# Kernel tuning notes

Measured on AMD Instinct MI355X. Metric: run time of the kernel, lower is better.

Reference implementation:

```python
import jax, jax.numpy as jnp
import numpy as np

B, N, D = 8, 2048, 1024

def setup_inputs() -> dict:
    key = jax.random.key(0)
    k1, k2, k3, k4 = jax.random.split(key, 4)
    q = jax.random.normal(k1, (B, N, D), dtype=jnp.float32)
    k = jax.random.normal(k2, (B, N, D), dtype=jnp.float32)
    v = jax.random.uniform(k3, (B, N, N), dtype=jnp.float32)
    # nn.Linear default init (kaiming-uniform-ish); scale is irrelevant for correctness
    bound = 1.0 / np.sqrt(D)
    W1 = jax.random.uniform(k4, (D, D), dtype=jnp.float32, minval=-bound, maxval=bound)
    b1 = jnp.zeros((D,), dtype=jnp.float32)
    return {"q": q, "k": k, "v": v, "W1": W1, "b1": b1}

def adj_normalization(adj):
    # D^{-1/2} A D^{-1/2} with rowsum clamped at 1; expressed as O(N^2)
    # broadcast scaling instead of the original's two diagonal bmms.
    rowsum = jnp.maximum(adj.sum(-1), 1.0)          # [B, N]
    d_inv_sqrt = rowsum ** -0.5                      # [B, N]
    return d_inv_sqrt[:, :, None] * adj * d_inv_sqrt[:, None, :]

def reference(q, k, v, W1, b1):
    # ff_layers == 1: q_out = linear1(q) (dropout is identity in eval);
    # k is unused because _fc returns (q_out, q_out).
    q_out = jnp.einsum('bnd,ed->bne', q, W1) + b1    # [B, N, D]
    attn = jnp.einsum('bnd,bmd->bnm', q_out, q_out)  # [B, N, N]
    # comb_mode == 2 (learn_n_norm): symmetric normalization of attn; v unused.
    output = adj_normalization(attn)
    return (output, attn)
```

## Files before the change

### kernel.cpp

```cpp
#include <hip/hip_runtime.h>

#define B_ 8
#define N_ 2048
#define D_ 1024

using u16 = unsigned short;
typedef __attribute__((ext_vector_type(8))) short short8;
typedef __attribute__((ext_vector_type(4))) float f32x4;
typedef __attribute__((ext_vector_type(4))) float float4v;
typedef __attribute__((ext_vector_type(4))) int int4v;

static __device__ __forceinline__ float bf2f(u16 h) {
  return __uint_as_float(((unsigned)h) << 16);
}
static __device__ __forceinline__ u16 f2bf(float f) {
  unsigned u = __float_as_uint(f);
  u += 0x7FFFu + ((u >> 16) & 1u);
  return (u16)(u >> 16);
}

static __device__ __forceinline__ void gload16(const void* g, void* l) {
  __builtin_amdgcn_global_load_lds((const __attribute__((address_space(1))) void*)g,
                                   (__attribute__((address_space(3))) void*)l, 16, 0, 0);
}

__global__ void cvt_f32_to_bf16(const float* __restrict__ in, u16* __restrict__ out, int n8) {
  const int stride = gridDim.x * blockDim.x;
  for (int i = blockIdx.x * blockDim.x + threadIdx.x; i < n8; i += stride) {
    const float4v* p = (const float4v*)in + (size_t)i * 2;
    float4v a = p[0], b = p[1];
    union { u16 h[8]; int4v v; } r;
    r.h[0] = f2bf(a.x); r.h[1] = f2bf(a.y); r.h[2] = f2bf(a.z); r.h[3] = f2bf(a.w);
    r.h[4] = f2bf(b.x); r.h[5] = f2bf(b.y); r.h[6] = f2bf(b.z); r.h[7] = f2bf(b.w);
    ((int4v*)out)[i] = r.v;
  }
}

__global__ __launch_bounds__(256, 2)
void gemm1_kernel(const u16* __restrict__ A, const u16* __restrict__ Bm,
                  const float* __restrict__ bias, u16* __restrict__ C,
                  int Nc, int K)
{
  const int lane = threadIdx.x & 63;
  const int wave = threadIdx.x >> 6;
  const int wr = wave >> 1, wc = wave & 1;
  const int tM = blockIdx.y << 7;
  const int tN = blockIdx.x << 7;

  __shared__ u16 As[128 * 32];
  __shared__ u16 Bs[128 * 32];

  const int srow = wave * 16 + (lane >> 2);
  const int scol = (lane & 3) * 8;
  const u16* ga0 = A  + (size_t)(tM + srow)      * K + scol;
  const u16* ga1 = A  + (size_t)(tM + srow + 64) * K + scol;
  const u16* gb0 = Bm + (size_t)(tN + srow)      * K + scol;
  const u16* gb1 = Bm + (size_t)(tN + srow + 64) * K + scol;
  u16* lA0 = As + wave * 512;
  u16* lA1 = As + 2048 + wave * 512;
  u16* lB0 = Bs + wave * 512;
  u16* lB1 = Bs + 2048 + wave * 512;

  f32x4 acc[4][4];
  #pragma unroll
  for (int m = 0; m < 4; ++m)
    #pragma unroll
    for (int n = 0; n < 4; ++n)
      acc[m][n] = (f32x4){0.f, 0.f, 0.f, 0.f};

  const int arow = wr * 64 + (lane & 15);
  const int brow = wc * 64 + (lane & 15);
  const int kblk = (lane >> 4) * 8;

  for (int k0 = 0; k0 < K; k0 += 32) {
    __syncthreads();
    gload16(ga0 + k0, lA0);
    gload16(ga1 + k0, lA1);
    gload16(gb0 + k0, lB0);
    gload16(gb1 + k0, lB1);
    asm volatile("s_waitcnt vmcnt(0)" ::: "memory");
    __syncthreads();

    short8 af[4], bfr[4];
    #pragma unroll
    for (int m = 0; m < 4; ++m)
      af[m] = *(const short8*)(As + (arow + m * 16) * 32 + kblk);
    #pragma unroll
    for (int n = 0; n < 4; ++n)
      bfr[n] = *(const short8*)(Bs + (brow + n * 16) * 32 + kblk);

    #pragma unroll
    for (int m = 0; m < 4; ++m)
      #pragma unroll
      for (int n = 0; n < 4; ++n)
        acc[m][n] = __builtin_amdgcn_mfma_f32_16x16x32_bf16(af[m], bfr[n], acc[m][n], 0, 0, 0);
  }

  const int r0 = tM + wr * 64 + (lane >> 4) * 4;
  const int c0 = tN + wc * 64 + (lane & 15);
  #pragma unroll
  for (int m = 0; m < 4; ++m)
    #pragma unroll
    for (int n = 0; n < 4; ++n) {
      const int col = c0 + n * 16;
      const float bv = bias[col];
      #pragma unroll
      for (int j = 0; j < 4; ++j)
        C[(size_t)(r0 + m * 16 + j) * Nc + col] = f2bf(acc[m][n][j] + bv);
    }
}

__global__ __launch_bounds__(256, 2)
void gemm2_fused(const u16* __restrict__ Qbase, const float* __restrict__ dinv,
                 float* __restrict__ attnBase, float* __restrict__ outBase)
{
  const int z = blockIdx.z;
  const u16* A = Qbase + (size_t)z * N_ * D_;
  const int lane = threadIdx.x & 63;
  const int wave = threadIdx.x >> 6;
  const int wr = wave >> 1, wc = wave & 1;
  const int tM = blockIdx.y << 7;
  const int tN = blockIdx.x << 7;

  __shared__ u16 As[128 * 32];
  __shared__ u16 Bs[128 * 32];

  const int srow = wave * 16 + (lane >> 2);
  const int scol = (lane & 3) * 8;
  const u16* ga0 = A + (size_t)(tM + srow)      * D_ + scol;
  const u16* ga1 = A + (size_t)(tM + srow + 64) * D_ + scol;
  const u16* gb0 = A + (size_t)(tN + srow)      * D_ + scol;
  const u16* gb1 = A + (size_t)(tN + srow + 64) * D_ + scol;
  u16* lA0 = As + wave * 512;
  u16* lA1 = As + 2048 + wave * 512;
  u16* lB0 = Bs + wave * 512;
  u16* lB1 = Bs + 2048 + wave * 512;

  f32x4 acc[4][4];
  #pragma unroll
  for (int m = 0; m < 4; ++m)
    #pragma unroll
    for (int n = 0; n < 4; ++n)
      acc[m][n] = (f32x4){0.f, 0.f, 0.f, 0.f};

  const int arow = wr * 64 + (lane & 15);
  const int brow = wc * 64 + (lane & 15);
  const int kblk = (lane >> 4) * 8;

  for (int k0 = 0; k0 < D_; k0 += 32) {
    __syncthreads();
    gload16(ga0 + k0, lA0);
    gload16(ga1 + k0, lA1);
    gload16(gb0 + k0, lB0);
    gload16(gb1 + k0, lB1);
    asm volatile("s_waitcnt vmcnt(0)" ::: "memory");
    __syncthreads();

    short8 af[4], bfr[4];
    #pragma unroll
    for (int m = 0; m < 4; ++m)
      af[m] = *(const short8*)(As + (arow + m * 16) * 32 + kblk);
    #pragma unroll
    for (int n = 0; n < 4; ++n)
      bfr[n] = *(const short8*)(Bs + (brow + n * 16) * 32 + kblk);

    #pragma unroll
    for (int m = 0; m < 4; ++m)
      #pragma unroll
      for (int n = 0; n < 4; ++n)
        acc[m][n] = __builtin_amdgcn_mfma_f32_16x16x32_bf16(af[m], bfr[n], acc[m][n], 0, 0, 0);
  }

  float* Cattn = attnBase + (size_t)z * N_ * N_;
  float* Cout  = outBase  + (size_t)z * N_ * N_;
  const float* dv = dinv + z * N_;

  const int r0 = tM + wr * 64 + (lane >> 4) * 4;
  const int c0 = tN + wc * 64 + (lane & 15);
  float di[4][4];
  #pragma unroll
  for (int m = 0; m < 4; ++m)
    #pragma unroll
    for (int j = 0; j < 4; ++j)
      di[m][j] = dv[r0 + m * 16 + j];

  #pragma unroll
  for (int m = 0; m < 4; ++m)
    #pragma unroll
    for (int n = 0; n < 4; ++n) {
      const int col = c0 + n * 16;
      const float dj = dv[col];
      #pragma unroll
      for (int j = 0; j < 4; ++j) {
        const size_t off = (size_t)(r0 + m * 16 + j) * N_ + col;
        const float a = acc[m][n][j];
        Cattn[off] = a;
        Cout[off]  = a * di[m][j] * dj;
      }
    }
}

__global__ void qsum_kernel(const float* __restrict__ q, float* __restrict__ qsum) {
  const int b   = blockIdx.z;
  const int d   = blockIdx.x * 256 + threadIdx.x;
  const int r0  = blockIdx.y * 256;
  const float* p = q + ((size_t)b * N_ + r0) * D_ + d;
  float acc = 0.f;
  for (int r = 0; r < 256; ++r) acc += p[(size_t)r * D_];
  atomicAdd(&qsum[b * D_ + d], acc);
}

__global__ void s_kernel(const float* __restrict__ qsum, const float* __restrict__ W1,
                         const float* __restrict__ b1, float* __restrict__ s) {
  const int idx = blockIdx.x * 256 + threadIdx.x;
  const int b = idx >> 10, e = idx & (D_ - 1);
  const int d0 = blockIdx.y * 256;
  const float4v* wp = (const float4v*)(W1 + (size_t)e * D_ + d0);
  const float4v* qp = (const float4v*)(qsum + b * D_ + d0);
  float acc = 0.f;
  #pragma unroll 4
  for (int t = 0; t < 64; ++t) {
    float4v w = wp[t], qv = qp[t];
    acc += w.x * qv.x + w.y * qv.y + w.z * qv.z + w.w * qv.w;
  }
  if (blockIdx.y == 0) acc += (float)N_ * b1[e];
  atomicAdd(&s[b * D_ + e], acc);
}

__global__ void t_kernel(const float* __restrict__ W1, const float* __restrict__ s,
                         float* __restrict__ tv) {
  const int idx = blockIdx.x * 256 + threadIdx.x;
  const int b = idx >> 10, d = idx & (D_ - 1);
  const int e0 = blockIdx.y * 256;
  const float* wp = W1 + (size_t)e0 * D_ + d;
  const float* sp = s + b * D_ + e0;
  float acc = 0.f;
  #pragma unroll 8
  for (int e = 0; e < 256; ++e) acc += wp[(size_t)e * D_] * sp[e];
  atomicAdd(&tv[b * D_ + d], acc);
}

__global__ void c_kernel(const float* __restrict__ b1, const float* __restrict__ s,
                         float* __restrict__ c) {
  const int b = blockIdx.x;
  const int tid = threadIdx.x;
  float acc = 0.f;
  #pragma unroll
  for (int t = 0; t < 4; ++t) {
    const int e = tid + t * 256;
    acc += b1[e] * s[b * D_ + e];
  }
  __shared__ float red[4];
  #pragma unroll
  for (int off = 32; off; off >>= 1) acc += __shfl_down(acc, off);
  if ((tid & 63) == 0) red[tid >> 6] = acc;
  __syncthreads();
  if (tid == 0) c[b] = red[0] + red[1] + red[2] + red[3];
}

__global__ void rowdinv_kernel(const float* __restrict__ q, const float* __restrict__ tv,
                               const float* __restrict__ c, float* __restrict__ dinv) {
  const int row  = blockIdx.x * 4 + (threadIdx.x >> 6);
  const int lane = threadIdx.x & 63;
  const int b    = row >> 11;
  const float4v* p  = (const float4v*)(q + (size_t)row * D_);
  const float4v* tp = (const float4v*)(tv + b * D_);
  float acc = 0.f;
  #pragma unroll
  for (int it = 0; it < 4; ++it) {
    float4v qv = p[it * 64 + lane];
    float4v tw = tp[it * 64 + lane];
    acc += qv.x * tw.x + qv.y * tw.y + qv.z * tw.z + qv.w * tw.w;
  }
  #pragma unroll
  for (int off = 32; off; off >>= 1) acc += __shfl_down(acc, off);
  if (lane == 0) dinv[row] = rsqrtf(fmaxf(acc + c[b], 1.0f));
}

extern "C" void kernel_launch(void* const* d_in, const int* in_sizes, int n_in,
                              void* d_out, int out_size, void* d_ws, size_t ws_size,
                              hipStream_t stream) {
  const float* q  = (const float*)d_in[0];
  const float* W1 = (const float*)d_in[3];
  const float* b1 = (const float*)d_in[4];

  float* out  = (float*)d_out;
  float* attn = out + (size_t)B_ * N_ * N_;

  char* ws = (char*)d_ws;
  u16*   qbf  = (u16*)ws;
  u16*   qout = (u16*)(ws + (size_t)33554432);
  u16*   w1bf = (u16*)(ws + (size_t)67108864);
  float* qsum = (float*)(ws + (size_t)69206016);
  float* s    = (float*)(ws + (size_t)69238784);
  float* tv   = (float*)(ws + (size_t)69271552);
  float* c    = (float*)(ws + (size_t)69304320);
  float* dinv = (float*)(ws + (size_t)69304576);

  hipMemsetAsync(qsum, 0, 3 * B_ * D_ * sizeof(float) + 256, stream);

  cvt_f32_to_bf16<<<2048, 256, 0, stream>>>(q, qbf, B_ * N_ * D_ / 8);
  cvt_f32_to_bf16<<<512, 256, 0, stream>>>(W1, w1bf, D_ * D_ / 8);

  dim3 g1(D_ / 128, (B_ * N_) / 128, 1);
  gemm1_kernel<<<g1, 256, 0, stream>>>(qbf, w1bf, b1, qout, D_, D_);

  qsum_kernel<<<dim3(D_ / 256, N_ / 256, B_), 256, 0, stream>>>(q, qsum);
  s_kernel<<<dim3(B_ * D_ / 256, 4), 256, 0, stream>>>(qsum, W1, b1, s);
  t_kernel<<<dim3(B_ * D_ / 256, 4), 256, 0, stream>>>(W1, s, tv);
  c_kernel<<<B_, 256, 0, stream>>>(b1, s, c);
  rowdinv_kernel<<<(B_ * N_) / 4, 256, 0, stream>>>(q, tv, c, dinv);

  dim3 g2(N_ / 128, N_ / 128, B_);
  gemm2_fused<<<g2, 256, 0, stream>>>(qout, dinv, attn, out);
}
```

Before: 244.1 us.

## Replace both GEMMs with a 256x256 double-buffered 8-wave kernel and fuse q conversion with qsum

Both GEMMs now go through one templated kernel that computes 256x256 output tiles with 8 waves. It uses a K-step of 64, double-buffered LDS filled by global_load_lds, XOR-swizzled LDS addressing, s_setprio around the MFMA bursts, and a remapped block order for L2 locality. Separately, the f32-to-bf16 conversion of q is fused with the column-sum reduction, so q is read once for both instead of twice. The aim is more data reuse per tile, overlap of loads with compute, and fewer bank conflicts. In exchange it uses more registers and LDS per block, and it hardcodes the problem sizes.

```diff
diff --git a/kernel.cpp b/kernel.cpp
--- a/kernel.cpp
+++ b/kernel.cpp
@@ -22,6 +22,204 @@
 static __device__ __forceinline__ void gload16(const void* g, void* l) {
   __builtin_amdgcn_global_load_lds((const __attribute__((address_space(1))) void*)g,
                                    (__attribute__((address_space(3))) void*)l, 16, 0, 0);
+}
+
+
+__device__ __forceinline__ void stage(u16* __restrict__ L,
+                                      const u16* __restrict__ gA,
+                                      const u16* __restrict__ gB,
+                                      int kof, int w) {
+  #pragma unroll
+  for (int i = 0; i < 4; ++i)
+    gload16(gA + (size_t)(i * 64) * 1024 + kof, L + i * 4096 + w * 512);
+  #pragma unroll
+  for (int i = 0; i < 4; ++i)
+    gload16(gB + (size_t)(i * 64) * 1024 + kof, L + 16384 + i * 4096 + w * 512);
+}
+
+__device__ __forceinline__ void ktile(const u16* __restrict__ Lb,
+                                      int wr, int wc, int lane15, int ck0,
+                                      f32x4 (&acc)[8][4]) {
+  const u16* Ar = Lb + (wr * 128 + lane15) * 64;
+  const u16* Br = Lb + 16384 + (wc * 64 + lane15) * 64;
+  const int ck1 = ck0 ^ 32;
+  short8 a[4], a2[4], b[4];
+
+  #pragma unroll
+  for (int m = 0; m < 4; ++m) a[m] = *(const short8*)(Ar + m * 1024 + ck0);
+  #pragma unroll
+  for (int n = 0; n < 4; ++n) b[n] = *(const short8*)(Br + n * 1024 + ck0);
+  __builtin_amdgcn_s_barrier();
+  __builtin_amdgcn_s_setprio(1);
+  #pragma unroll
+  for (int m = 0; m < 4; ++m)
+    #pragma unroll
+    for (int n = 0; n < 4; ++n)
+      acc[m][n] = __builtin_amdgcn_mfma_f32_16x16x32_bf16(a[m], b[n], acc[m][n], 0, 0, 0);
+  __builtin_amdgcn_s_setprio(0);
+  __builtin_amdgcn_s_barrier();
+
+  #pragma unroll
+  for (int m = 0; m < 4; ++m) a2[m] = *(const short8*)(Ar + (m + 4) * 1024 + ck0);
+  __builtin_amdgcn_s_barrier();
+  __builtin_amdgcn_s_setprio(1);
+  #pragma unroll
+  for (int m = 0; m < 4; ++m)
+    #pragma unroll
+    for (int n = 0; n < 4; ++n)
+      acc[m + 4][n] = __builtin_amdgcn_mfma_f32_16x16x32_bf16(a2[m], b[n], acc[m + 4][n], 0, 0, 0);
+  __builtin_amdgcn_s_setprio(0);
+  __builtin_amdgcn_s_barrier();
+
+  #pragma unroll
+  for (int m = 0; m < 4; ++m) a[m] = *(const short8*)(Ar + m * 1024 + ck1);
+  #pragma unroll
+  for (int n = 0; n < 4; ++n) b[n] = *(const short8*)(Br + n * 1024 + ck1);
+  __builtin_amdgcn_s_barrier();
+  __builtin_amdgcn_s_setprio(1);
+  #pragma unroll
+  for (int m = 0; m < 4; ++m)
+    #pragma unroll
+    for (int n = 0; n < 4; ++n)
+      acc[m][n] = __builtin_amdgcn_mfma_f32_16x16x32_bf16(a[m], b[n], acc[m][n], 0, 0, 0);
+  __builtin_amdgcn_s_setprio(0);
+  __builtin_amdgcn_s_barrier();
+
+  #pragma unroll
+  for (int m = 0; m < 4; ++m) a2[m] = *(const short8*)(Ar + (m + 4) * 1024 + ck1);
+  __builtin_amdgcn_s_barrier();
+  __builtin_amdgcn_s_setprio(1);
+  #pragma unroll
+  for (int m = 0; m < 4; ++m)
+    #pragma unroll
+    for (int n = 0; n < 4; ++n)
+      acc[m + 4][n] = __builtin_amdgcn_mfma_f32_16x16x32_bf16(a2[m], b[n], acc[m + 4][n], 0, 0, 0);
+  __builtin_amdgcn_s_setprio(0);
+  __builtin_amdgcn_s_barrier();
+}
+
+template<int MODE>
+__global__ __launch_bounds__(512, 2)
+void gemm8p(const u16* __restrict__ Abase, const u16* __restrict__ Bbase,
+            const float* __restrict__ aux,
+            void* __restrict__ C0, float* __restrict__ C1)
+{
+  __shared__ u16 lds[2][32768];
+  const int tid = threadIdx.x;
+  const int w = tid >> 6, l = tid & 63;
+
+  int tm0, tn0, z = 0;
+  if (MODE == 0) {
+    const int bid = blockIdx.x;
+    const int s = (bid & 7) * 32 + (bid >> 3);
+    tm0 = (s >> 2) << 8;
+    tn0 = (s & 3) << 8;
+  } else {
+    const int bid = blockIdx.x;
+    const int s = (bid & 7) * 64 + (bid >> 3);
+    z  = s >> 6;
+    tm0 = ((s >> 3) & 7) << 8;
+    tn0 = (s & 7) << 8;
+  }
+  const u16* A  = Abase + (MODE ? (size_t)z * N_ * D_ : 0);
+  const u16* Bm = (MODE ? A : Bbase);
+
+  const int sr = w * 8 + (l >> 3);
+  const int sc = (((l & 7) ^ (l >> 3)) << 4) >> 1;
+  const u16* gA = A  + (size_t)(tm0 + sr) * 1024 + sc;
+  const u16* gB = Bm + (size_t)(tn0 + sr) * 1024 + sc;
+
+  const int lane15 = l & 15, lhi = l >> 4;
+  const int ck0 = ((lhi << 4) ^ ((l & 7) << 4)) >> 1;
+  const int wr = w >> 2, wc = w & 3;
+
+  f32x4 acc[8][4];
+  #pragma unroll
+  for (int m = 0; m < 8; ++m)
+    #pragma unroll
+    for (int n = 0; n < 4; ++n)
+      acc[m][n] = (f32x4){0.f, 0.f, 0.f, 0.f};
+
+  stage(&lds[0][0], gA, gB, 0, w);
+  stage(&lds[1][0], gA, gB, 64, w);
+
+  for (int t = 0; t < 16; t += 2) {
+    asm volatile("s_waitcnt vmcnt(8)" ::: "memory");
+    __builtin_amdgcn_s_barrier();
+    ktile(&lds[0][0], wr, wc, lane15, ck0, acc);
+    stage(&lds[0][0], gA, gB, ((t + 2) & 15) * 64, w);
+    asm volatile("s_waitcnt vmcnt(8)" ::: "memory");
+    __builtin_amdgcn_s_barrier();
+    ktile(&lds[1][0], wr, wc, lane15, ck0, acc);
+    stage(&lds[1][0], gA, gB, ((t + 3) & 15) * 64, w);
+  }
+  asm volatile("s_waitcnt vmcnt(0)" ::: "memory");
+
+  const int rbase = tm0 + wr * 128 + lhi * 4;
+  const int cbase = tn0 + wc * 64 + lane15;
+
+  if (MODE == 0) {
+    u16* C = (u16*)C0;
+    #pragma unroll
+    for (int m = 0; m < 8; ++m)
+      #pragma unroll
+      for (int n = 0; n < 4; ++n) {
+        const int col = cbase + n * 16;
+        const float bv = aux[col];
+        #pragma unroll
+        for (int j = 0; j < 4; ++j)
+          C[(size_t)(rbase + m * 16 + j) * 1024 + col] = f2bf(acc[m][n][j] + bv);
+      }
+  } else {
+    float* Cattn = (float*)C0 + (size_t)z * N_ * N_;
+    float* Cout  = C1 + (size_t)z * N_ * N_;
+    const float* dv = aux + z * N_;
+    float di[8][4];
+    #pragma unroll
+    for (int m = 0; m < 8; ++m)
+      #pragma unroll
+      for (int j = 0; j < 4; ++j)
+        di[m][j] = dv[rbase + m * 16 + j];
+    #pragma unroll
+    for (int m = 0; m < 8; ++m)
+      #pragma unroll
+      for (int n = 0; n < 4; ++n) {
+        const int col = cbase + n * 16;
+        const float dj = dv[col];
+        #pragma unroll
+        for (int j = 0; j < 4; ++j) {
+          const size_t off = (size_t)(rbase + m * 16 + j) * N_ + col;
+          const float a = acc[m][n][j];
+          Cattn[off] = a;
+          Cout[off]  = a * di[m][j] * dj;
+        }
+      }
+  }
+}
+
+__global__ void cvt_q_qsum(const float* __restrict__ q, u16* __restrict__ qbf,
+                           float* __restrict__ qsum) {
+  const int wi = blockIdx.x * 256 + threadIdx.x;
+  const int d0 = (wi & 127) * 8;
+  const int rc = (wi >> 7) & 63;
+  const int b  = wi >> 13;
+  const size_t base = ((size_t)b * N_ + rc * 32) * D_ + d0;
+  float s[8];
+  #pragma unroll
+  for (int k = 0; k < 8; ++k) s[k] = 0.f;
+  for (int r = 0; r < 32; ++r) {
+    const float4v* p = (const float4v*)(q + base + (size_t)r * D_);
+    float4v x = p[0], y = p[1];
+    union { u16 h[8]; int4v v; } o;
+    o.h[0] = f2bf(x.x); o.h[1] = f2bf(x.y); o.h[2] = f2bf(x.z); o.h[3] = f2bf(x.w);
+    o.h[4] = f2bf(y.x); o.h[5] = f2bf(y.y); o.h[6] = f2bf(y.z); o.h[7] = f2bf(y.w);
+    *(int4v*)(qbf + base + (size_t)r * D_) = o.v;
+    s[0] += x.x; s[1] += x.y; s[2] += x.z; s[3] += x.w;
+    s[4] += y.x; s[5] += y.y; s[6] += y.z; s[7] += y.w;
+  }
+  float* qs = qsum + b * D_ + d0;
+  #pragma unroll
+  for (int k = 0; k < 8; ++k) atomicAdd(qs + k, s[k]);
 }
 
 __global__ void cvt_f32_to_bf16(const float* __restrict__ in, u16* __restrict__ out, int n8) {
@@ -34,180 +232,6 @@
     r.h[4] = f2bf(b.x); r.h[5] = f2bf(b.y); r.h[6] = f2bf(b.z); r.h[7] = f2bf(b.w);
     ((int4v*)out)[i] = r.v;
   }
-}
-
-__global__ __launch_bounds__(256, 2)
-void gemm1_kernel(const u16* __restrict__ A, const u16* __restrict__ Bm,
-                  const float* __restrict__ bias, u16* __restrict__ C,
-                  int Nc, int K)
-{
-  const int lane = threadIdx.x & 63;
-  const int wave = threadIdx.x >> 6;
-  const int wr = wave >> 1, wc = wave & 1;
-  const int tM = blockIdx.y << 7;
-  const int tN = blockIdx.x << 7;
-
-  __shared__ u16 As[128 * 32];
-  __shared__ u16 Bs[128 * 32];
-
-  const int srow = wave * 16 + (lane >> 2);
-  const int scol = (lane & 3) * 8;
-  const u16* ga0 = A  + (size_t)(tM + srow)      * K + scol;
-  const u16* ga1 = A  + (size_t)(tM + srow + 64) * K + scol;
-  const u16* gb0 = Bm + (size_t)(tN + srow)      * K + scol;
-  const u16* gb1 = Bm + (size_t)(tN + srow + 64) * K + scol;
-  u16* lA0 = As + wave * 512;
-  u16* lA1 = As + 2048 + wave * 512;
-  u16* lB0 = Bs + wave * 512;
-  u16* lB1 = Bs + 2048 + wave * 512;
-
-  f32x4 acc[4][4];
-  #pragma unroll
-  for (int m = 0; m < 4; ++m)
-    #pragma unroll
-    for (int n = 0; n < 4; ++n)
-      acc[m][n] = (f32x4){0.f, 0.f, 0.f, 0.f};
-
-  const int arow = wr * 64 + (lane & 15);
-  const int brow = wc * 64 + (lane & 15);
-  const int kblk = (lane >> 4) * 8;
-
-  for (int k0 = 0; k0 < K; k0 += 32) {
-    __syncthreads();
-    gload16(ga0 + k0, lA0);
-    gload16(ga1 + k0, lA1);
-    gload16(gb0 + k0, lB0);
-    gload16(gb1 + k0, lB1);
-    asm volatile("s_waitcnt vmcnt(0)" ::: "memory");
-    __syncthreads();
-
-    short8 af[4], bfr[4];
-    #pragma unroll
-    for (int m = 0; m < 4; ++m)
-      af[m] = *(const short8*)(As + (arow + m * 16) * 32 + kblk);
-    #pragma unroll
-    for (int n = 0; n < 4; ++n)
-      bfr[n] = *(const short8*)(Bs + (brow + n * 16) * 32 + kblk);
-
-    #pragma unroll
-    for (int m = 0; m < 4; ++m)
-      #pragma unroll
-      for (int n = 0; n < 4; ++n)
-        acc[m][n] = __builtin_amdgcn_mfma_f32_16x16x32_bf16(af[m], bfr[n], acc[m][n], 0, 0, 0);
-  }
-
-  const int r0 = tM + wr * 64 + (lane >> 4) * 4;
-  const int c0 = tN + wc * 64 + (lane & 15);
-  #pragma unroll
-  for (int m = 0; m < 4; ++m)
-    #pragma unroll
-    for (int n = 0; n < 4; ++n) {
-      const int col = c0 + n * 16;
-      const float bv = bias[col];
-      #pragma unroll
-      for (int j = 0; j < 4; ++j)
-        C[(size_t)(r0 + m * 16 + j) * Nc + col] = f2bf(acc[m][n][j] + bv);
-    }
-}
-
-__global__ __launch_bounds__(256, 2)
-void gemm2_fused(const u16* __restrict__ Qbase, const float* __restrict__ dinv,
-                 float* __restrict__ attnBase, float* __restrict__ outBase)
-{
-  const int z = blockIdx.z;
-  const u16* A = Qbase + (size_t)z * N_ * D_;
-  const int lane = threadIdx.x & 63;
-  const int wave = threadIdx.x >> 6;
-  const int wr = wave >> 1, wc = wave & 1;
-  const int tM = blockIdx.y << 7;
-  const int tN = blockIdx.x << 7;
-
-  __shared__ u16 As[128 * 32];
-  __shared__ u16 Bs[128 * 32];
-
-  const int srow = wave * 16 + (lane >> 2);
-  const int scol = (lane & 3) * 8;
-  const u16* ga0 = A + (size_t)(tM + srow)      * D_ + scol;
-  const u16* ga1 = A + (size_t)(tM + srow + 64) * D_ + scol;
-  const u16* gb0 = A + (size_t)(tN + srow)      * D_ + scol;
-  const u16* gb1 = A + (size_t)(tN + srow + 64) * D_ + scol;
-  u16* lA0 = As + wave * 512;
-  u16* lA1 = As + 2048 + wave * 512;
-  u16* lB0 = Bs + wave * 512;
-  u16* lB1 = Bs + 2048 + wave * 512;
-
-  f32x4 acc[4][4];
-  #pragma unroll
-  for (int m = 0; m < 4; ++m)
-    #pragma unroll
-    for (int n = 0; n < 4; ++n)
-      acc[m][n] = (f32x4){0.f, 0.f, 0.f, 0.f};
-
-  const int arow = wr * 64 + (lane & 15);
-  const int brow = wc * 64 + (lane & 15);
-  const int kblk = (lane >> 4) * 8;
-
-  for (int k0 = 0; k0 < D_; k0 += 32) {
-    __syncthreads();
-    gload16(ga0 + k0, lA0);
-    gload16(ga1 + k0, lA1);
-    gload16(gb0 + k0, lB0);
-    gload16(gb1 + k0, lB1);
-    asm volatile("s_waitcnt vmcnt(0)" ::: "memory");
-    __syncthreads();
-
-    short8 af[4], bfr[4];
-    #pragma unroll
-    for (int m = 0; m < 4; ++m)
-      af[m] = *(const short8*)(As + (arow + m * 16) * 32 + kblk);
-    #pragma unroll
-    for (int n = 0; n < 4; ++n)
-      bfr[n] = *(const short8*)(Bs + (brow + n * 16) * 32 + kblk);
-
-    #pragma unroll
-    for (int m = 0; m < 4; ++m)
-      #pragma unroll
-      for (int n = 0; n < 4; ++n)
-        acc[m][n] = __builtin_amdgcn_mfma_f32_16x16x32_bf16(af[m], bfr[n], acc[m][n], 0, 0, 0);
-  }
-
-  float* Cattn = attnBase + (size_t)z * N_ * N_;
-  float* Cout  = outBase  + (size_t)z * N_ * N_;
-  const float* dv = dinv + z * N_;
-
-  const int r0 = tM + wr * 64 + (lane >> 4) * 4;
-  const int c0 = tN + wc * 64 + (lane & 15);
-  float di[4][4];
-  #pragma unroll
-  for (int m = 0; m < 4; ++m)
-    #pragma unroll
-    for (int j = 0; j < 4; ++j)
-      di[m][j] = dv[r0 + m * 16 + j];
-
-  #pragma unroll
-  for (int m = 0; m < 4; ++m)
-    #pragma unroll
-    for (int n = 0; n < 4; ++n) {
-      const int col = c0 + n * 16;
-      const float dj = dv[col];
-      #pragma unroll
-      for (int j = 0; j < 4; ++j) {
-        const size_t off = (size_t)(r0 + m * 16 + j) * N_ + col;
-        const float a = acc[m][n][j];
-        Cattn[off] = a;
-        Cout[off]  = a * di[m][j] * dj;
-      }
-    }
-}
-
-__global__ void qsum_kernel(const float* __restrict__ q, float* __restrict__ qsum) {
-  const int b   = blockIdx.z;
-  const int d   = blockIdx.x * 256 + threadIdx.x;
-  const int r0  = blockIdx.y * 256;
-  const float* p = q + ((size_t)b * N_ + r0) * D_ + d;
-  float acc = 0.f;
-  for (int r = 0; r < 256; ++r) acc += p[(size_t)r * D_];
-  atomicAdd(&qsum[b * D_ + d], acc);
 }
 
 __global__ void s_kernel(const float* __restrict__ qsum, const float* __restrict__ W1,
@@ -220,8 +244,8 @@
   float acc = 0.f;
   #pragma unroll 4
   for (int t = 0; t < 64; ++t) {
-    float4v w = wp[t], qv = qp[t];
-    acc += w.x * qv.x + w.y * qv.y + w.z * qv.z + w.w * qv.w;
+    float4v wv = wp[t], qv = qp[t];
+    acc += wv.x * qv.x + wv.y * qv.y + wv.z * qv.z + wv.w * qv.w;
   }
   if (blockIdx.y == 0) acc += (float)N_ * b1[e];
   atomicAdd(&s[b * D_ + e], acc);
@@ -299,18 +323,15 @@
 
   hipMemsetAsync(qsum, 0, 3 * B_ * D_ * sizeof(float) + 256, stream);
 
-  cvt_f32_to_bf16<<<2048, 256, 0, stream>>>(q, qbf, B_ * N_ * D_ / 8);
+  cvt_q_qsum<<<256, 256, 0, stream>>>(q, qbf, qsum);
   cvt_f32_to_bf16<<<512, 256, 0, stream>>>(W1, w1bf, D_ * D_ / 8);
 
-  dim3 g1(D_ / 128, (B_ * N_) / 128, 1);
-  gemm1_kernel<<<g1, 256, 0, stream>>>(qbf, w1bf, b1, qout, D_, D_);
-
-  qsum_kernel<<<dim3(D_ / 256, N_ / 256, B_), 256, 0, stream>>>(q, qsum);
+  gemm8p<0><<<256, 512, 0, stream>>>(qbf, w1bf, b1, qout, nullptr);
+
   s_kernel<<<dim3(B_ * D_ / 256, 4), 256, 0, stream>>>(qsum, W1, b1, s);
   t_kernel<<<dim3(B_ * D_ / 256, 4), 256, 0, stream>>>(W1, s, tv);
   c_kernel<<<B_, 256, 0, stream>>>(b1, s, c);
   rowdinv_kernel<<<(B_ * N_) / 4, 256, 0, stream>>>(q, tv, c, dinv);
 
-  dim3 g2(N_ / 128, N_ / 128, B_);
-  gemm2_fused<<<g2, 256, 0, stream>>>(qout, dinv, attn, out);
-}
+  gemm8p<1><<<512, 512, 0, stream>>>(qout, nullptr, dinv, attn, out);
+}
```

New measurement: 216.3 us, median of 2. 1.13x faster.
